# Optimization experiments

Measured on AMD Instinct MI355X. Metric: run time of the kernel, lower is better.

Reference implementation:

```python
import jax, jax.numpy as jnp
import numpy as np

DECAY = 0.99
EPS = 1e-05
TEMP = 1.0


def setup_inputs() -> dict:
    key = jax.random.key(0)
    k1, k2, k3 = jax.random.split(key, 3)
    B, T, D, C = 64, 512, 256, 1024
    x = jax.random.normal(k1, (B, T, D), dtype=jnp.float32)
    embed = jax.random.normal(k2, (1, C, D), dtype=jnp.float32)
    embed_avg = jax.random.normal(k3, (1, C, D), dtype=jnp.float32)
    cluster_size = jnp.ones((1, C), dtype=jnp.float32)
    return {"x": x, "embed": embed, "embed_avg": embed_avg, "cluster_size": cluster_size}


def reference(x, embed, embed_avg, cluster_size):
    B, T, D = x.shape
    H, C, _ = embed.shape  # H = num_codebooks = 1
    flatten = x.reshape(H, B * T, D)  # pack_one 'h * d'
    e = jax.lax.stop_gradient(embed)  # learnable_codebook = False

    dist = (2.0 * jnp.einsum('hnd,hcd->hnc', flatten, e)
            - jnp.sum(flatten * flatten, axis=-1, keepdims=True)
            - jnp.sum(e * e, axis=-1)[:, None, :])  # [h, N, C]

    # gumbel_sample: deterministic argmax + straight-through one-hot
    embed_ind = jnp.argmax(dist, axis=-1)  # [h, N]
    probs = jax.nn.softmax(dist / TEMP, axis=-1)
    hard = jax.nn.one_hot(embed_ind, C, dtype=dist.dtype)
    embed_onehot = probs + jax.lax.stop_gradient(hard - probs)  # [h, N, C]

    # quantize via onehot matmul (training path)
    quantize = jnp.einsum('hnc,hcd->hnd', embed_onehot, e).reshape(B, T, D)

    # EMA codebook update
    cs_new = DECAY * cluster_size + (1.0 - DECAY) * embed_onehot.sum(axis=1)  # [h, C]
    embed_sum = jnp.einsum('hnd,hnc->hcd', flatten, embed_onehot)  # [h, C, D]
    ea_new = DECAY * embed_avg + (1.0 - DECAY) * embed_sum
    n = jnp.sum(cs_new, axis=-1, keepdims=True)
    cs_smoothed = (cs_new + EPS) / (n + C * EPS) * n  # laplace smoothing * n
    embed_norm = ea_new / cs_smoothed[..., None]  # new codebook [h, C, D]

    return (quantize, embed_ind.reshape(B, T), embed_norm, cs_new)
```

## Files before the change

kernel.cpp:

```cpp
#include <hip/hip_runtime.h>
#include <cstdint>

#define DECAY 0.99f
#define OMD   0.01f
#define EPSV  1e-5f

constexpr int N_PTS   = 32768;
constexpr int D_DIM   = 256;
constexpr int C_CODES = 1024;
constexpr int NKT     = 12;
constexpr int AP      = 256;
constexpr int BP      = 512;

constexpr int PG = 8;
constexpr int PK = 8;
constexpr int LCAP = 4096;

typedef _Float16 half8  __attribute__((ext_vector_type(8)));
typedef _Float16 half4v __attribute__((ext_vector_type(4)));
typedef float    floatx4 __attribute__((ext_vector_type(4)));

constexpr size_t WS_ENORM = 0;
constexpr size_t WS_FCNT  = 1024;
constexpr size_t WS_XNORM = 2048;
constexpr size_t WS_PCNT  = 34816;
constexpr size_t WS_CAND4 = 43008;
constexpr size_t WS_FLAGR = WS_CAND4 + 1048576;
constexpr size_t WS_KEY64 = WS_FLAGR + 32768;
constexpr size_t WS_A16   = WS_KEY64 + 65536;
constexpr size_t WS_B16   = WS_A16 + 4194304;
constexpr size_t WS_TOTAL_FLOATS = WS_B16 + 262144;

__device__ __forceinline__ void async_copy16(const void* g, void* s) {
    __builtin_amdgcn_global_load_lds(
        (const __attribute__((address_space(1))) unsigned int*)(uintptr_t)g,
        (__attribute__((address_space(3))) unsigned int*)(uintptr_t)s, 16, 0, 0);
}

__device__ __forceinline__ unsigned ord_u32(float v) {
    unsigned s = __float_as_uint(v);
    unsigned m = (unsigned)((int)s >> 31);
    return s ^ (m | 0x80000000u);
}
__device__ __forceinline__ float ord_dec(unsigned t) {
    unsigned s = (t & 0x80000000u) ? (t ^ 0x80000000u) : ~t;
    return __uint_as_float(s);
}

__device__ __forceinline__ _Float16 lo_h(float f) {
    _Float16 h = (_Float16)f;
    return (_Float16)(f - (float)h);
}

__global__ __launch_bounds__(256) void vq_prep(const float* __restrict__ X,
                                               const float* __restrict__ E,
                                               _Float16* __restrict__ A,
                                               _Float16* __restrict__ B,
                                               float* __restrict__ enorm,
                                               float* __restrict__ xnorm,
                                               int* __restrict__ fcnt) {
    if (blockIdx.x < 8192) {
        int i = blockIdx.x * 256 + threadIdx.x;
        int n = i >> 6, kq = (i & 63) * 4;
        float4 v = reinterpret_cast<const float4*>(X)[i];
        _Float16 h0 = (_Float16)v.x, h1 = (_Float16)v.y, h2 = (_Float16)v.z, h3 = (_Float16)v.w;
        half4v hi = {h0, h1, h2, h3};
        *reinterpret_cast<half4v*>(A + (size_t)n * AP + kq) = hi;
        float s = v.x * v.x + v.y * v.y + v.z * v.z + v.w * v.w;
        int lane = threadIdx.x & 63;
#pragma unroll
        for (int off = 32; off > 0; off >>= 1) s += __shfl_down(s, off, 64);
        if (lane == 0) xnorm[n] = s;
    } else {
        if (blockIdx.x == 8192 && threadIdx.x == 0) *fcnt = 0;
        int i = (blockIdx.x - 8192) * 256 + threadIdx.x;
        int c = i >> 6, kq = (i & 63) * 4;
        float4 v = reinterpret_cast<const float4*>(E)[i];
        _Float16 h0 = (_Float16)v.x, h1 = (_Float16)v.y, h2 = (_Float16)v.z, h3 = (_Float16)v.w;
        _Float16 l0 = lo_h(v.x), l1 = lo_h(v.y), l2 = lo_h(v.z), l3 = lo_h(v.w);
        half4v hi = {h0, h1, h2, h3};
        half4v lo = {l0, l1, l2, l3};
        _Float16* row = B + (size_t)c * BP;
        *reinterpret_cast<half4v*>(row + kq)       = hi;
        *reinterpret_cast<half4v*>(row + 256 + kq) = lo;
        float s = v.x * v.x + v.y * v.y + v.z * v.z + v.w * v.w;
        int lane = threadIdx.x & 63;
#pragma unroll
        for (int off = 32; off > 0; off >>= 1) s += __shfl_down(s, off, 64);
        if (lane == 0) enorm[c] = s;
    }
}

__global__ __launch_bounds__(256) void vq_enorm(const float* __restrict__ E,
                                                float* __restrict__ enorm) {
    int c    = blockIdx.x * 4 + (threadIdx.x >> 6);
    int lane = threadIdx.x & 63;
    float4 v = reinterpret_cast<const float4*>(E)[c * 64 + lane];
    float s  = v.x * v.x + v.y * v.y + v.z * v.z + v.w * v.w;
#pragma unroll
    for (int off = 32; off > 0; off >>= 1) s += __shfl_down(s, off, 64);
    if (lane == 0) enorm[c] = s;
}

#define TOP2_DPP(CTRL)                                                          \
    {                                                                           \
        unsigned o1 = (unsigned)__builtin_amdgcn_update_dpp((int)k1, (int)k1,   \
                                                            CTRL, 0xF, 0xF, false); \
        unsigned o2 = (unsigned)__builtin_amdgcn_update_dpp((int)k2, (int)k2,   \
                                                            CTRL, 0xF, 0xF, false); \
        unsigned tmn = o1 < k1 ? o1 : k1;                                       \
        k1 = o1 > k1 ? o1 : k1;                                                 \
        k2 = o2 > k2 ? o2 : k2;                                                 \
        k2 = tmn > k2 ? tmn : k2;                                               \
    }

__global__ __launch_bounds__(256, 2) void vq_gemm1(
    const _Float16* __restrict__ A, const _Float16* __restrict__ B,
    const float* __restrict__ enorm, float4* __restrict__ cand4) {
    __shared__ _Float16 As[128 * 64];
    __shared__ _Float16 Bs[256 * 64];

    const int L  = blockIdx.x;
    const int ct = (L >> 3) & 3;
    const int rt = (L & 7) | ((L >> 5) << 3);
    const int n0  = rt * 128;
    const int cb0 = ct * 256;

    const int tid = threadIdx.x;
    const int w   = tid >> 6;
    const int l   = tid & 63;

    const int srow = l >> 3;
    const int sq   = (l & 7) ^ srow;

    floatx4 acc[4][8] = {};

    for (int kt = 0; kt < 4; ++kt) {
        const int k0 = kt * 64;
        __syncthreads();
#pragma unroll
        for (int t = 0; t < 4; ++t) {
            int rr = w * 32 + t * 8;
            const _Float16* ga = A + (size_t)(n0 + rr + srow) * AP + k0 + sq * 8;
            async_copy16(ga, &As[rr * 64]);
        }
#pragma unroll
        for (int t = 0; t < 8; ++t) {
            int rr = w * 64 + t * 8;
            const _Float16* gb = B + (size_t)(cb0 + rr + srow) * BP + k0 + sq * 8;
            async_copy16(gb, &Bs[rr * 64]);
        }
        __syncthreads();
#pragma unroll
        for (int kk = 0; kk < 2; ++kk) {
            half8 af[4], bf[8];
            int qa = kk * 4 + (l >> 4);
#pragma unroll
            for (int i = 0; i < 4; ++i) {
                int row = (w & 1) * 64 + 16 * i + (l & 15);
                af[i] = *reinterpret_cast<const half8*>(&As[row * 64 + (qa ^ (row & 7)) * 8]);
            }
#pragma unroll
            for (int j = 0; j < 8; ++j) {
                int crow = (w >> 1) * 128 + 16 * j + (l & 15);
                bf[j] = *reinterpret_cast<const half8*>(&Bs[crow * 64 + (qa ^ (crow & 7)) * 8]);
            }
#pragma unroll
            for (int i = 0; i < 4; ++i)
#pragma unroll
                for (int j = 0; j < 8; ++j)
                    acc[i][j] = __builtin_amdgcn_mfma_f32_16x16x32_f16(af[i], bf[j], acc[i][j], 0, 0, 0);
        }
    }

    const int colbase = cb0 + (w >> 1) * 128 + (l & 15);
    float    en[8];
    unsigned idxenc[8];
#pragma unroll
    for (int j = 0; j < 8; ++j) {
        en[j]     = enorm[colbase + 16 * j];
        idxenc[j] = 1023u - (unsigned)(colbase + 16 * j);
    }

#pragma unroll
    for (int i = 0; i < 4; ++i) {
#pragma unroll
        for (int reg = 0; reg < 4; ++reg) {
            unsigned k1 = 0u, k2 = 0u;
#pragma unroll
            for (int j = 0; j < 8; ++j) {
                float v = 2.0f * acc[i][j][reg] - en[j];
                unsigned key = (ord_u32(v) & 0xFFFFFC00u) | idxenc[j];
                unsigned tmn = key < k1 ? key : k1;
                k1 = key > k1 ? key : k1;
                k2 = tmn > k2 ? tmn : k2;
            }
            TOP2_DPP(0xB1)
            TOP2_DPP(0x4E)
            TOP2_DPP(0x141)
            TOP2_DPP(0x140)
            if ((l & 15) == 0) {
                unsigned c1 = 1023u - (k1 & 1023u);
                float v1 = ord_dec(k1 & 0xFFFFFC00u);
                float v2 = ord_dec(k2 & 0xFFFFFC00u);
                int row = n0 + (w & 1) * 64 + 16 * i + (l >> 4) * 4 + reg;
                cand4[(size_t)row * 8 + ct * 2 + (w >> 1)] =
                    make_float4(v1, (float)c1, v2, 0.0f);
            }
        }
    }
}

__global__ __launch_bounds__(256) void vq_merge3f(
    const float4* __restrict__ cand4, const float* __restrict__ E,
    const float* __restrict__ enorm, const float* __restrict__ xnorm,
    float* __restrict__ quant, float* __restrict__ indout,
    int* __restrict__ flagrows, int* __restrict__ fcnt,
    unsigned long long* __restrict__ keyarr) {
    __shared__ int   rowsel[64];
    __shared__ float emred[256];
    const int tid = threadIdx.x;
    const int n0  = blockIdx.x * 64;

    float em = fmaxf(fmaxf(enorm[tid], enorm[tid + 256]),
                     fmaxf(enorm[tid + 512], enorm[tid + 768]));
    emred[tid] = em;
    __syncthreads();
    for (int st = 128; st > 0; st >>= 1) {
        if (tid < st) emred[tid] = fmaxf(emred[tid], emred[tid + st]);
        __syncthreads();
    }
    const float emax = emred[0];

    if (tid < 64) {
        int r = n0 + tid;
        float b1 = -3.4e38f, b2 = -3.4e38f;
        int   i1 = 0x7fffffff;
#pragma unroll
        for (int t = 0; t < 8; ++t) {
            float4 cv = cand4[(size_t)r * 8 + t];
            int ci = (int)cv.y;
            if (cv.x > b1 || (cv.x == b1 && ci < i1)) { b2 = fmaxf(b1, cv.z); b1 = cv.x; i1 = ci; }
            else b2 = fmaxf(b2, cv.x);
        }
        i1 &= (C_CODES - 1);
        rowsel[tid] = i1;
        indout[r]   = (float)i1;
        float T = 0.004150390625f * sqrtf(xnorm[r] * emax)
                + 0.0001220703125f * emax + 0.5f;
        if (b1 - b2 <= T) {
            int p = atomicAdd(fcnt, 1);
            flagrows[p] = r;
            keyarr[p]   = 0ull;
        }
    }
    __syncthreads();

    const float4* E4 = reinterpret_cast<const float4*>(E);
    float4*       Q4 = reinterpret_cast<float4*>(quant);
    const int lane = tid & 63;
#pragma unroll
    for (int it = 0; it < 16; ++it) {
        int r   = (tid >> 6) + 4 * it;
        int idx = rowsel[r];
        Q4[(n0 + r) * 64 + lane] = E4[idx * 64 + lane];
    }
}

__global__ __launch_bounds__(256, 2) void vq_gemm2(
    const _Float16* __restrict__ A, const _Float16* __restrict__ B,
    const float* __restrict__ X, const float* __restrict__ enorm,
    const int* __restrict__ flagrows, const int* __restrict__ fcnt,
    unsigned long long* __restrict__ keyarr) {
    const int fc = *fcnt;

    const int L      = blockIdx.x;
    const int within = L >> 3;
    const int ct     = within & 7;
    const int rt     = (L & 7) | ((within >> 3) << 3);
    const int n0     = rt * 128;
    if (n0 >= fc) return;
    const int cb0    = ct * 128;

    __shared__ _Float16 As[128 * 64];
    __shared__ _Float16 Bs[128 * 64];

    const int tid = threadIdx.x;
    const int w   = tid >> 6;
    const int l   = tid & 63;
    const int srow = l >> 3;
    const int sq   = (l & 7) ^ srow;

    int grow[4];
#pragma unroll
    for (int t = 0; t < 4; ++t) {
        int slot = n0 + w * 32 + t * 8 + srow;
        int r    = (slot < fc) ? flagrows[slot] : 0;
        grow[t]  = r & (N_PTS - 1);
    }

    floatx4 acc[4][4] = {};

    for (int kt = 0; kt < NKT; ++kt) {
        const int ka = ((kt < 8) ? (kt & 3) : (kt - 4)) * 64;
        const int kb = (kt < 4) ? kt * 64 : (kt < 8 ? 256 + (kt - 4) * 64 : (kt - 8) * 64);
        __syncthreads();
        if (kt < 8) {
#pragma unroll
            for (int t = 0; t < 4; ++t) {
                int rr = w * 32 + t * 8;
                const _Float16* ga = A + (size_t)grow[t] * AP + ka + sq * 8;
                async_copy16(ga, &As[rr * 64]);
                const _Float16* gb = B + (size_t)(cb0 + rr + srow) * BP + kb + sq * 8;
                async_copy16(gb, &Bs[rr * 64]);
            }
        } else {
            const int kx = ka - 256;
#pragma unroll
            for (int t = 0; t < 4; ++t) {
                int rr = w * 32 + t * 8;
                const float* xr = X + (size_t)grow[t] * D_DIM + kx + sq * 8;
                float4 xa = *reinterpret_cast<const float4*>(xr);
                float4 xb = *reinterpret_cast<const float4*>(xr + 4);
                half8 hv;
                hv[0] = lo_h(xa.x); hv[1] = lo_h(xa.y); hv[2] = lo_h(xa.z); hv[3] = lo_h(xa.w);
                hv[4] = lo_h(xb.x); hv[5] = lo_h(xb.y); hv[6] = lo_h(xb.z); hv[7] = lo_h(xb.w);
                *reinterpret_cast<half8*>(&As[rr * 64 + l * 8]) = hv;
                const _Float16* gb = B + (size_t)(cb0 + rr + srow) * BP + kb + sq * 8;
                async_copy16(gb, &Bs[rr * 64]);
            }
        }
        __syncthreads();
#pragma unroll
        for (int kk = 0; kk < 2; ++kk) {
            half8 af[4], bf[4];
            int qa = kk * 4 + (l >> 4);
#pragma unroll
            for (int i = 0; i < 4; ++i) {
                int row  = (w & 1) * 64 + 16 * i + (l & 15);
                af[i] = *reinterpret_cast<const half8*>(&As[row * 64 + (qa ^ (row & 7)) * 8]);
                int crow = (w >> 1) * 64 + 16 * i + (l & 15);
                bf[i] = *reinterpret_cast<const half8*>(&Bs[crow * 64 + (qa ^ (crow & 7)) * 8]);
            }
#pragma unroll
            for (int i = 0; i < 4; ++i)
#pragma unroll
                for (int j = 0; j < 4; ++j)
                    acc[i][j] = __builtin_amdgcn_mfma_f32_16x16x32_f16(af[i], bf[j], acc[i][j], 0, 0, 0);
        }
    }

    const int colbase = cb0 + (w >> 1) * 64 + (l & 15);
    float en[4];
#pragma unroll
    for (int j = 0; j < 4; ++j) en[j] = enorm[colbase + 16 * j];

#pragma unroll
    for (int i = 0; i < 4; ++i) {
#pragma unroll
        for (int reg = 0; reg < 4; ++reg) {
            float bv = -3.4e38f;
            int   bi = 0x7fffffff;
#pragma unroll
            for (int j = 0; j < 4; ++j) {
                float v = 2.0f * acc[i][j][reg] - en[j];
                int   c = colbase + 16 * j;
                if (v > bv || (v == bv && c < bi)) { bv = v; bi = c; }
            }
#pragma unroll
            for (int s = 1; s < 16; s <<= 1) {
                float ov = __shfl_xor(bv, s, 64);
                int   oi = __shfl_xor(bi, s, 64);
                if (ov > bv || (ov == bv && oi < bi)) { bv = ov; bi = oi; }
            }
            if ((l & 15) == 0) {
                int slot = n0 + (w & 1) * 64 + 16 * i + (l >> 4) * 4 + reg;
                unsigned long long key =
                    ((unsigned long long)ord_u32(bv) << 10) | (1023u - (unsigned)bi);
                atomicMax(&keyarr[slot], key);
            }
        }
    }
}

__global__ __launch_bounds__(256) void vq_patch(
    const unsigned long long* __restrict__ keyarr, const int* __restrict__ flagrows,
    const int* __restrict__ fcnt, const float* __restrict__ E,
    float* __restrict__ quant, float* __restrict__ indout) {
    int fc = *fcnt;
    if (fc > N_PTS) fc = N_PTS;
    const int s0 = blockIdx.x * 64;
    if (s0 >= fc) return;

    __shared__ int rowsel[64];
    __shared__ int rowid[64];
    const int tid = threadIdx.x;
    if (tid < 64) {
        int s = s0 + tid;
        if (s < fc) {
            unsigned long long k = keyarr[s];
            int c = (int)(1023u - (unsigned)(k & 1023u)) & (C_CODES - 1);
            int r = flagrows[s] & (N_PTS - 1);
            rowsel[tid] = c;
            rowid[tid]  = r;
            indout[r]   = (float)c;
        } else {
            rowsel[tid] = -1;
            rowid[tid]  = 0;
        }
    }
    __syncthreads();

    const float4* E4 = reinterpret_cast<const float4*>(E);
    float4*       Q4 = reinterpret_cast<float4*>(quant);
    const int lane = tid & 63;
#pragma unroll
    for (int it = 0; it < 16; ++it) {
        int rs  = (tid >> 6) + 4 * it;
        int idx = rowsel[rs];
        if (idx >= 0) Q4[(size_t)rowid[rs] * 64 + lane] = E4[idx * 64 + lane];
    }
}

__global__ __launch_bounds__(256) void vq_part(
    const float* __restrict__ X, const float* __restrict__ indf,
    float* __restrict__ P, int* __restrict__ pcnt) {
    __shared__ int list[LCAP];
    __shared__ int cnt[PK];
    __shared__ int lcnt;
    const int cg = blockIdx.x;
    const int g  = blockIdx.y;
    const int t  = threadIdx.x;
    if (t == 0) lcnt = 0;
    if (t < PK) cnt[t] = 0;
    __syncthreads();

    const float4* I4 = reinterpret_cast<const float4*>(indf);
    float4 v[4];
#pragma unroll
    for (int j = 0; j < 4; ++j)
        v[j] = I4[g * 1024 + j * 256 + t];

#pragma unroll
    for (int j = 0; j < 4; ++j) {
        int base = (g * 1024 + j * 256 + t) * 4;
        int k0 = (int)v[j].x, k1 = (int)v[j].y, k2 = (int)v[j].z, k3 = (int)v[j].w;
        if ((k0 >> 3) == cg) { int p = atomicAdd(&lcnt, 1); atomicAdd(&cnt[k0 & 7], 1); if (p < LCAP) list[p] = ((base + 0) << 3) | (k0 & 7); }
        if ((k1 >> 3) == cg) { int p = atomicAdd(&lcnt, 1); atomicAdd(&cnt[k1 & 7], 1); if (p < LCAP) list[p] = ((base + 1) << 3) | (k1 & 7); }
        if ((k2 >> 3) == cg) { int p = atomicAdd(&lcnt, 1); atomicAdd(&cnt[k2 & 7], 1); if (p < LCAP) list[p] = ((base + 2) << 3) | (k2 & 7); }
        if ((k3 >> 3) == cg) { int p = atomicAdd(&lcnt, 1); atomicAdd(&cnt[k3 & 7], 1); if (p < LCAP) list[p] = ((base + 3) << 3) | (k3 & 7); }
    }
    __syncthreads();

    int m = lcnt; if (m > LCAP) m = LCAP;
    float acc[PK] = {0, 0, 0, 0, 0, 0, 0, 0};
    int r = 0;
    for (; r + 8 <= m; r += 8) {
        int e[8];
        float val[8];
#pragma unroll
        for (int q = 0; q < 8; ++q) e[q] = list[r + q];
#pragma unroll
        for (int q = 0; q < 8; ++q) val[q] = X[(size_t)(e[q] >> 3) * D_DIM + t];
#pragma unroll
        for (int q = 0; q < 8; ++q) {
            int k = e[q] & 7;
#pragma unroll
            for (int kk = 0; kk < PK; ++kk) acc[kk] += (k == kk) ? val[q] : 0.0f;
        }
    }
    for (; r < m; ++r) {
        int e = list[r];
        float val = X[(size_t)(e >> 3) * D_DIM + t];
        int k = e & 7;
#pragma unroll
        for (int kk = 0; kk < PK; ++kk) acc[kk] += (k == kk) ? val : 0.0f;
    }

#pragma unroll
    for (int kk = 0; kk < PK; ++kk)
        P[((size_t)g * C_CODES + cg * PK + kk) * D_DIM + t] = acc[kk];
    if (t < PK) pcnt[g * C_CODES + cg * PK + t] = cnt[t];
}

__global__ __launch_bounds__(256) void vq_comb(
    const float* __restrict__ P, const int* __restrict__ pcnt,
    const float* __restrict__ ea, const float* __restrict__ cs_in,
    float* __restrict__ emb_norm, float* __restrict__ cs_out) {
    __shared__ float red[256];
    const int c = blockIdx.x;
    const int t = threadIdx.x;
    red[t] = cs_in[t] + cs_in[t + 256] + cs_in[t + 512] + cs_in[t + 768];
    __syncthreads();
    for (int st = 128; st > 0; st >>= 1) {
        if (t < st) red[t] += red[t + st];
        __syncthreads();
    }
    const float cssum = red[0];

    float s = 0.0f;
#pragma unroll
    for (int g = 0; g < PG; ++g)
        s += P[((size_t)g * C_CODES + c) * D_DIM + t];
    int total = 0;
#pragma unroll
    for (int g = 0; g < PG; ++g) total += pcnt[g * C_CODES + c];
    float cs    = DECAY * cs_in[c] + OMD * (float)total;
    float ntot  = DECAY * cssum + OMD * (float)N_PTS;
    float denom = (cs + EPSV) / (ntot + (float)C_CODES * EPSV) * ntot;
    emb_norm[(size_t)c * D_DIM + t] =
        (DECAY * ea[(size_t)c * D_DIM + t] + OMD * s) / denom;
    if (t == 0) cs_out[c] = cs;
}

__global__ __launch_bounds__(256) void vq_main_fb(
    const float* __restrict__ X, const float* __restrict__ E,
    const float* __restrict__ enorm,
    float* __restrict__ quant, float* __restrict__ indout,
    float* __restrict__ counts, float* __restrict__ esum) {
    constexpr int BN = 64, BC = 64, BK = 32, PADR = 68;
    __shared__ float As[BK * PADR];
    __shared__ float Bs[BK * PADR];
    __shared__ float redv[BN * 16];
    __shared__ int   redi[BN * 16];
    __shared__ int   rowsel[BN];

    const int tid = threadIdx.x;
    const int n0  = blockIdx.x * BN;
    const int tr  = tid >> 4;
    const int tc  = tid & 15;
    const int sr  = tid >> 2;
    const int sk  = tid & 3;

    const float4* X4 = reinterpret_cast<const float4*>(X);
    const float4* E4 = reinterpret_cast<const float4*>(E);

    float best[4];
    int   bidx[4];
#pragma unroll
    for (int i = 0; i < 4; i++) { best[i] = -3.4e38f; bidx[i] = 0; }

    for (int c0 = 0; c0 < C_CODES; c0 += BC) {
        float acc[4][4] = {};
        for (int k0 = 0; k0 < D_DIM; k0 += BK) {
            __syncthreads();
#pragma unroll
            for (int it = 0; it < 2; ++it) {
                int   k4 = sk + 4 * it;
                float4 av = X4[(n0 + sr) * 64 + (k0 >> 2) + k4];
                float4 bv = E4[(c0 + sr) * 64 + (k0 >> 2) + k4];
                int kk = k4 * 4;
                As[(kk + 0) * PADR + sr] = av.x;
                As[(kk + 1) * PADR + sr] = av.y;
                As[(kk + 2) * PADR + sr] = av.z;
                As[(kk + 3) * PADR + sr] = av.w;
                Bs[(kk + 0) * PADR + sr] = bv.x;
                Bs[(kk + 1) * PADR + sr] = bv.y;
                Bs[(kk + 2) * PADR + sr] = bv.z;
                Bs[(kk + 3) * PADR + sr] = bv.w;
            }
            __syncthreads();
#pragma unroll
            for (int k = 0; k < BK; ++k) {
                float4 a = *reinterpret_cast<const float4*>(&As[k * PADR + 4 * tr]);
                float4 b = *reinterpret_cast<const float4*>(&Bs[k * PADR + 4 * tc]);
                acc[0][0] += a.x * b.x; acc[0][1] += a.x * b.y;
                acc[0][2] += a.x * b.z; acc[0][3] += a.x * b.w;
                acc[1][0] += a.y * b.x; acc[1][1] += a.y * b.y;
                acc[1][2] += a.y * b.z; acc[1][3] += a.y * b.w;
                acc[2][0] += a.z * b.x; acc[2][1] += a.z * b.y;
                acc[2][2] += a.z * b.z; acc[2][3] += a.z * b.w;
                acc[3][0] += a.w * b.x; acc[3][1] += a.w * b.y;
                acc[3][2] += a.w * b.z; acc[3][3] += a.w * b.w;
            }
        }
        float4 en = *reinterpret_cast<const float4*>(&enorm[c0 + 4 * tc]);
        float enj[4] = {en.x, en.y, en.z, en.w};
#pragma unroll
        for (int i = 0; i < 4; i++)
#pragma unroll
            for (int j = 0; j < 4; j++) {
                float v = 2.0f * acc[i][j] - enj[j];
                int   c = c0 + 4 * tc + j;
                if (v > best[i]) { best[i] = v; bidx[i] = c; }
            }
    }

    __syncthreads();
#pragma unroll
    for (int i = 0; i < 4; i++) {
        redv[(4 * tr + i) * 16 + tc] = best[i];
        redi[(4 * tr + i) * 16 + tc] = bidx[i];
    }
    __syncthreads();
    if (tid < BN) {
        float bv = redv[tid * 16];
        int   bi = redi[tid * 16];
        for (int t = 1; t < 16; t++) {
            float v  = redv[tid * 16 + t];
            int   id = redi[tid * 16 + t];
            if (v > bv || (v == bv && id < bi)) { bv = v; bi = id; }
        }
        rowsel[tid] = bi;
        indout[n0 + tid] = (float)bi;
        unsafeAtomicAdd(&counts[bi], 1.0f);
    }
    __syncthreads();

    float4*   Q4   = reinterpret_cast<float4*>(quant);
    const int lane = tid & 63;
#pragma unroll
    for (int it = 0; it < 16; ++it) {
        int r   = (tid >> 6) + 4 * it;
        int idx = rowsel[r];
        float4 ev = E4[idx * 64 + lane];
        Q4[(n0 + r) * 64 + lane] = ev;
        float4 xv = X4[(n0 + r) * 64 + lane];
        float* dst = &esum[idx * D_DIM + lane * 4];
        unsafeAtomicAdd(dst + 0, xv.x);
        unsafeAtomicAdd(dst + 1, xv.y);
        unsafeAtomicAdd(dst + 2, xv.z);
        unsafeAtomicAdd(dst + 3, xv.w);
    }
}

__global__ __launch_bounds__(1024) void vq_fin1(const float* __restrict__ cs_in,
                                                const float* __restrict__ counts,
                                                float* __restrict__ cs_out,
                                                float* __restrict__ denom) {
    __shared__ float red[1024];
    int   c  = threadIdx.x;
    float cs = DECAY * cs_in[c] + OMD * counts[c];
    cs_out[c] = cs;
    red[c]    = cs;
    __syncthreads();
    for (int s = 512; s > 0; s >>= 1) {
        if (c < s) red[c] += red[c + s];
        __syncthreads();
    }
    float ntot = red[0];
    denom[c] = (cs + EPSV) / (ntot + (float)C_CODES * EPSV) * ntot;
}

__global__ __launch_bounds__(256) void vq_fin2(const float* __restrict__ ea,
                                               const float* __restrict__ esum,
                                               const float* __restrict__ denom,
                                               float* __restrict__ out) {
    int i = blockIdx.x * 256 + threadIdx.x;
    int c = i >> 6;
    float4 a = reinterpret_cast<const float4*>(ea)[i];
    float4 s = reinterpret_cast<const float4*>(esum)[i];
    float  d = denom[c];
    float4 o;
    o.x = (DECAY * a.x + OMD * s.x) / d;
    o.y = (DECAY * a.y + OMD * s.y) / d;
    o.z = (DECAY * a.z + OMD * s.z) / d;
    o.w = (DECAY * a.w + OMD * s.w) / d;
    reinterpret_cast<float4*>(out)[i] = o;
}

extern "C" void kernel_launch(void* const* d_in, const int* in_sizes, int n_in,
                              void* d_out, int out_size, void* d_ws, size_t ws_size,
                              hipStream_t stream) {
    const float* x            = (const float*)d_in[0];
    const float* embed        = (const float*)d_in[1];
    const float* embed_avg    = (const float*)d_in[2];
    const float* cluster_size = (const float*)d_in[3];

    float* out      = (float*)d_out;
    float* quant    = out;
    float* ind      = out + (size_t)N_PTS * D_DIM;
    float* emb_norm = ind + N_PTS;
    float* cs_out   = emb_norm + (size_t)C_CODES * D_DIM;

    float* ws    = (float*)d_ws;
    float* enorm = ws + WS_ENORM;

    if (ws_size >= WS_TOTAL_FLOATS * sizeof(float)) {
        int*      fcnt  = (int*)(ws + WS_FCNT);
        int*      pcnt  = (int*)(ws + WS_PCNT);
        float*    xnorm = ws + WS_XNORM;
        float4*   cand4 = (float4*)(ws + WS_CAND4);
        int*      flagr = (int*)(ws + WS_FLAGR);
        unsigned long long* key64 = (unsigned long long*)(ws + WS_KEY64);
        _Float16* A16   = (_Float16*)(ws + WS_A16);
        _Float16* B16   = (_Float16*)(ws + WS_B16);
        float*    P     = ws + WS_A16;

        vq_prep<<<8448, 256, 0, stream>>>(x, embed, A16, B16, enorm, xnorm, fcnt);
        vq_gemm1<<<1024, 256, 0, stream>>>(A16, B16, enorm, cand4);
        vq_merge3f<<<N_PTS / 64, 256, 0, stream>>>(cand4, embed, enorm, xnorm,
                                                   quant, ind, flagr, fcnt, key64);
        vq_gemm2<<<2048, 256, 0, stream>>>(A16, B16, x, enorm, flagr, fcnt, key64);
        vq_patch<<<N_PTS / 64, 256, 0, stream>>>(key64, flagr, fcnt, embed, quant, ind);
        vq_part<<<dim3(C_CODES / PK, PG), 256, 0, stream>>>(x, ind, P, pcnt);
        vq_comb<<<C_CODES, 256, 0, stream>>>(P, pcnt, embed_avg, cluster_size,
                                             emb_norm, cs_out);
    } else {
        vq_enorm<<<C_CODES / 4, 256, 0, stream>>>(embed, enorm);
        float* countsf = ws + WS_CAND4;
        float* esum    = ws + WS_CAND4 + 1024;
        float* denom   = ws + WS_A16;
        hipMemsetAsync(countsf, 0, (1024 + (size_t)C_CODES * D_DIM) * sizeof(float), stream);
        vq_main_fb<<<N_PTS / 64, 256, 0, stream>>>(x, embed, enorm, quant, ind, countsf, esum);
        vq_fin1<<<1, 1024, 0, stream>>>(cluster_size, countsf, cs_out, denom);
        vq_fin2<<<(C_CODES * D_DIM / 4) / 256, 256, 0, stream>>>(embed_avg, esum, denom, emb_norm);
    }
}
```

Before: 200.2 us.

## Precompute fp16 low residual of x in prep; double partition groups in vq_part

The prep kernel now writes both the fp16 high part and the fp16 low residual of x into a wider A buffer. This lets the refinement GEMM load all A tiles with async global-to-LDS copies instead of reading fp32 x and converting it inline. The partition kernel also splits points into twice as many groups, with a smaller per-block list capacity, to raise parallelism. In exchange, prep writes twice as much A data and the workspace grows, and the smaller list cap risks overflow for heavily used codes.

```diff
diff --git a/kernel.cpp b/kernel.cpp
--- a/kernel.cpp
+++ b/kernel.cpp
@@ -9,12 +9,12 @@
 constexpr int D_DIM   = 256;
 constexpr int C_CODES = 1024;
 constexpr int NKT     = 12;
-constexpr int AP      = 256;
+constexpr int AP      = 512;
 constexpr int BP      = 512;
 
-constexpr int PG = 8;
+constexpr int PG = 16;
 constexpr int PK = 8;
-constexpr int LCAP = 4096;
+constexpr int LCAP = 2048;
 
 typedef _Float16 half8  __attribute__((ext_vector_type(8)));
 typedef _Float16 half4v __attribute__((ext_vector_type(4)));
@@ -24,11 +24,11 @@
 constexpr size_t WS_FCNT  = 1024;
 constexpr size_t WS_XNORM = 2048;
 constexpr size_t WS_PCNT  = 34816;
-constexpr size_t WS_CAND4 = 43008;
+constexpr size_t WS_CAND4 = 51200;
 constexpr size_t WS_FLAGR = WS_CAND4 + 1048576;
 constexpr size_t WS_KEY64 = WS_FLAGR + 32768;
 constexpr size_t WS_A16   = WS_KEY64 + 65536;
-constexpr size_t WS_B16   = WS_A16 + 4194304;
+constexpr size_t WS_B16   = WS_A16 + 8388608;
 constexpr size_t WS_TOTAL_FLOATS = WS_B16 + 262144;
 
 __device__ __forceinline__ void async_copy16(const void* g, void* s) {
@@ -64,8 +64,12 @@
         int n = i >> 6, kq = (i & 63) * 4;
         float4 v = reinterpret_cast<const float4*>(X)[i];
         _Float16 h0 = (_Float16)v.x, h1 = (_Float16)v.y, h2 = (_Float16)v.z, h3 = (_Float16)v.w;
+        _Float16 l0 = lo_h(v.x), l1 = lo_h(v.y), l2 = lo_h(v.z), l3 = lo_h(v.w);
         half4v hi = {h0, h1, h2, h3};
-        *reinterpret_cast<half4v*>(A + (size_t)n * AP + kq) = hi;
+        half4v lo = {l0, l1, l2, l3};
+        _Float16* row = A + (size_t)n * AP;
+        *reinterpret_cast<half4v*>(row + kq)       = hi;
+        *reinterpret_cast<half4v*>(row + 256 + kq) = lo;
         float s = v.x * v.x + v.y * v.y + v.z * v.z + v.w * v.w;
         int lane = threadIdx.x & 63;
 #pragma unroll
@@ -269,9 +273,8 @@
 
 __global__ __launch_bounds__(256, 2) void vq_gemm2(
     const _Float16* __restrict__ A, const _Float16* __restrict__ B,
-    const float* __restrict__ X, const float* __restrict__ enorm,
-    const int* __restrict__ flagrows, const int* __restrict__ fcnt,
-    unsigned long long* __restrict__ keyarr) {
+    const float* __restrict__ enorm, const int* __restrict__ flagrows,
+    const int* __restrict__ fcnt, unsigned long long* __restrict__ keyarr) {
     const int fc = *fcnt;
 
     const int L      = blockIdx.x;
@@ -305,30 +308,13 @@
         const int ka = ((kt < 8) ? (kt & 3) : (kt - 4)) * 64;
         const int kb = (kt < 4) ? kt * 64 : (kt < 8 ? 256 + (kt - 4) * 64 : (kt - 8) * 64);
         __syncthreads();
-        if (kt < 8) {
-#pragma unroll
-            for (int t = 0; t < 4; ++t) {
-                int rr = w * 32 + t * 8;
-                const _Float16* ga = A + (size_t)grow[t] * AP + ka + sq * 8;
-                async_copy16(ga, &As[rr * 64]);
-                const _Float16* gb = B + (size_t)(cb0 + rr + srow) * BP + kb + sq * 8;
-                async_copy16(gb, &Bs[rr * 64]);
-            }
-        } else {
-            const int kx = ka - 256;
-#pragma unroll
-            for (int t = 0; t < 4; ++t) {
-                int rr = w * 32 + t * 8;
-                const float* xr = X + (size_t)grow[t] * D_DIM + kx + sq * 8;
-                float4 xa = *reinterpret_cast<const float4*>(xr);
-                float4 xb = *reinterpret_cast<const float4*>(xr + 4);
-                half8 hv;
-                hv[0] = lo_h(xa.x); hv[1] = lo_h(xa.y); hv[2] = lo_h(xa.z); hv[3] = lo_h(xa.w);
-                hv[4] = lo_h(xb.x); hv[5] = lo_h(xb.y); hv[6] = lo_h(xb.z); hv[7] = lo_h(xb.w);
-                *reinterpret_cast<half8*>(&As[rr * 64 + l * 8]) = hv;
-                const _Float16* gb = B + (size_t)(cb0 + rr + srow) * BP + kb + sq * 8;
-                async_copy16(gb, &Bs[rr * 64]);
-            }
+#pragma unroll
+        for (int t = 0; t < 4; ++t) {
+            int rr = w * 32 + t * 8;
+            const _Float16* ga = A + (size_t)grow[t] * AP + ka + sq * 8;
+            async_copy16(ga, &As[rr * 64]);
+            const _Float16* gb = B + (size_t)(cb0 + rr + srow) * BP + kb + sq * 8;
+            async_copy16(gb, &Bs[rr * 64]);
         }
         __syncthreads();
 #pragma unroll
@@ -436,14 +422,14 @@
     __syncthreads();
 
     const float4* I4 = reinterpret_cast<const float4*>(indf);
-    float4 v[4];
-#pragma unroll
-    for (int j = 0; j < 4; ++j)
-        v[j] = I4[g * 1024 + j * 256 + t];
-
-#pragma unroll
-    for (int j = 0; j < 4; ++j) {
-        int base = (g * 1024 + j * 256 + t) * 4;
+    float4 v[2];
+#pragma unroll
+    for (int j = 0; j < 2; ++j)
+        v[j] = I4[g * 512 + j * 256 + t];
+
+#pragma unroll
+    for (int j = 0; j < 2; ++j) {
+        int base = (g * 512 + j * 256 + t) * 4;
         int k0 = (int)v[j].x, k1 = (int)v[j].y, k2 = (int)v[j].z, k3 = (int)v[j].w;
         if ((k0 >> 3) == cg) { int p = atomicAdd(&lcnt, 1); atomicAdd(&cnt[k0 & 7], 1); if (p < LCAP) list[p] = ((base + 0) << 3) | (k0 & 7); }
         if ((k1 >> 3) == cg) { int p = atomicAdd(&lcnt, 1); atomicAdd(&cnt[k1 & 7], 1); if (p < LCAP) list[p] = ((base + 1) << 3) | (k1 & 7); }
@@ -691,7 +677,7 @@
         vq_gemm1<<<1024, 256, 0, stream>>>(A16, B16, enorm, cand4);
         vq_merge3f<<<N_PTS / 64, 256, 0, stream>>>(cand4, embed, enorm, xnorm,
                                                    quant, ind, flagr, fcnt, key64);
-        vq_gemm2<<<2048, 256, 0, stream>>>(A16, B16, x, enorm, flagr, fcnt, key64);
+        vq_gemm2<<<2048, 256, 0, stream>>>(A16, B16, enorm, flagr, fcnt, key64);
         vq_patch<<<N_PTS / 64, 256, 0, stream>>>(key64, flagr, fcnt, embed, quant, ind);
         vq_part<<<dim3(C_CODES / PK, PG), 256, 0, stream>>>(x, ind, P, pcnt);
         vq_comb<<<C_CODES, 256, 0, stream>>>(P, pcnt, embed_avg, cluster_size,
```

New measurement: 192.8 us, median of 2. -3.7%, faster.
